# Performance work log

Measured on AMD Instinct MI355X. Metric: run time of the kernel, lower is better.

The kernel has to match this reference:

```python
import jax, jax.numpy as jnp
import numpy as np
import math

B, CIN, CH, H, W = 4, 64, 32, 64, 64
M_CH, DEPTH, K = 4, 3, 8
NPF = CIN // 2  # num_pos_feats per axis; pos channels = 2*NPF = CIN
TEMPERATURE = 10000.0


def sine_pos(h, w, npf, temperature=TEMPERATURE):
    # PositionEmbeddingSine with normalize=False; cumsum of ones == arange(1, n+1)
    y_embed = jnp.arange(1, h + 1, dtype=jnp.float32)
    x_embed = jnp.arange(1, w + 1, dtype=jnp.float32)
    dim_t = jnp.arange(npf, dtype=jnp.float32)
    dim_t = temperature ** (2.0 * jnp.floor(dim_t / 2.0) / npf)
    pos_x = jnp.broadcast_to(x_embed[None, :, None] / dim_t, (h, w, npf))
    pos_y = jnp.broadcast_to(y_embed[:, None, None] / dim_t, (h, w, npf))

    def interleave(p):
        return jnp.stack([jnp.sin(p[..., 0::2]), jnp.cos(p[..., 1::2])], axis=-1).reshape(h, w, npf)

    pos = jnp.concatenate([interleave(pos_y), interleave(pos_x)], axis=-1)  # (h,w,2*npf)
    return jnp.transpose(pos, (2, 0, 1))  # (2*npf, h, w)


def conv2d(x, wgt, bias, pad):
    y = jax.lax.conv_general_dilated(
        x, wgt, window_strides=(1, 1), padding=[(pad, pad), (pad, pad)],
        dimension_numbers=('NCHW', 'OIHW', 'NCHW'))
    return y + bias[None, :, None, None]


def setup_inputs() -> dict:
    key = jax.random.key(0)
    ks = jax.random.split(key, 13)
    s = 0.05
    return {
        'f':    jax.random.normal(ks[0], (B, CH, H, W), jnp.float32),
        'map':  jax.random.normal(ks[1], (B, 1, 32, 32), jnp.float32),
        'f_q':  jax.random.normal(ks[2], (B, CIN, H, W), jnp.float32),
        'f_k':  jax.random.normal(ks[3], (B, CIN, H, W), jnp.float32),
        'm_k':  jax.random.normal(ks[4], (B, 1, 32, 32), jnp.float32),
        'wq':   jax.random.normal(ks[5], (M_CH, CIN), jnp.float32) * s,
        'wk':   jax.random.normal(ks[6], (M_CH, CIN), jnp.float32) * s,
        'w_in':  jax.random.normal(ks[7], (CH, CH, 1, 1), jnp.float32) * s,
        'b_in':  jax.random.normal(ks[8], (CH,), jnp.float32) * s,
        'w_mid': jax.random.normal(ks[9], (DEPTH, CH, CH, 3, 3), jnp.float32) * s,
        'b_mid': jax.random.normal(ks[10], (DEPTH, CH), jnp.float32) * s,
        'w_out': jax.random.normal(ks[11], (1, CH, 3, 3), jnp.float32) * s,
        'b_out': jax.random.normal(ks[12], (1,), jnp.float32) * s,
    }


def reference(f, map, f_q, f_k, m_k, wq, wk, w_in, b_in, w_mid, b_mid, w_out, b_out):
    b, c, h, w = f_q.shape
    hf, wf = f.shape[2], f.shape[3]
    # self.ret: bilinear resize to f's spatial size (align_corners=False)
    map_r = jax.image.resize(map, (b, 1, hf, wf), method='bilinear')
    m_k_r = jax.image.resize(m_k, (b, 1, hf, wf), method='bilinear')

    pos = sine_pos(h, w, NPF)[None]  # (1, CIN, h, w); same for pos_emb_h/pos_emb_l
    fq_emb = f_q + pos
    fk_emb = f_k + pos

    # 1x1 convs == channel matmuls
    query = jnp.einsum('mc,bchw->bhwm', wq, fq_emb).reshape(b, h * w, M_CH)  # (b, N, m)
    key_t = jnp.einsum('mc,bchw->bmhw', wk, fk_emb).reshape(b, M_CH, h * w)  # (b, m, N)

    sim = jnp.einsum('bqm,bmk->bqk', query, key_t)   # (b, N, N)
    sim = jax.nn.softmax(sim, axis=-2)                # softmax over query axis (dim=-2)

    value = (jnp.exp(m_k_r) / math.e).reshape(b, 1, h * w)  # broadcast over query axis
    context = sim * value
    context_k, _ = jax.lax.top_k(context, K)          # (b, N, K) over last (key) axis
    context_m = jnp.mean(context_k, axis=-1)          # (b, N)
    corrected_map = context_m.reshape(b, 1, h, w)

    corrected_map = corrected_map * map_r + map_r
    rmap = 1.0 - jax.nn.sigmoid(corrected_map)

    x = rmap * f  # broadcast over channel dim
    x = conv2d(x, w_in, b_in, 0)
    for i in range(DEPTH):
        x = jax.nn.relu(conv2d(x, w_mid[i], b_mid[i], 1))
    out = conv2d(x, w_out, b_out, 1) + corrected_map
    return (x, out, corrected_map)
```

## Files before the change

kernel.cpp:

```cpp
#include <hip/hip_runtime.h>
#include <hip/hip_bf16.h>
#include <math.h>

#define BB 4
#define CIN 64
#define CH 32
#define NN 4096
#define NQCH 32
#define LOG2E 1.4426950408889634f
#define L2_10K 13.287712379549449f

#define Q4_OFF     1024
#define K4_OFF     66560
#define CV_OFF     132096
#define RMAP_OFF   148480
#define CMAPF_OFF  164864
#define CPSUM_OFF  181248
#define T8_OFF     705536
#define XA_OFF     4899840
#define XB_OFF     5424128

#define OUT_X_OFF   0
#define OUT_O_OFF   524288
#define OUT_CM_OFF  540672

#define CE(x, y) { float ce_lo = fminf(x, y); y = fmaxf(x, y); x = ce_lo; }
#define CED(x, y) { float ce_hi = fmaxf(x, y); y = fminf(x, y); x = ce_hi; }

#define SORT8(a0,a1,a2,a3,a4,a5,a6,a7) \
    CE(a0,a1); CE(a2,a3); CE(a4,a5); CE(a6,a7); \
    CE(a0,a2); CE(a1,a3); CE(a4,a6); CE(a5,a7); \
    CE(a1,a2); CE(a5,a6); \
    CE(a0,a4); CE(a1,a5); CE(a2,a6); CE(a3,a7); \
    CE(a2,a4); CE(a3,a5); \
    CE(a1,a2); CE(a3,a4); CE(a5,a6);

#define BITONIC8(a0,a1,a2,a3,a4,a5,a6,a7) \
    CE(a0,a4); CE(a1,a5); CE(a2,a6); CE(a3,a7); \
    CE(a0,a2); CE(a1,a3); CE(a4,a6); CE(a5,a7); \
    CE(a0,a1); CE(a2,a3); CE(a4,a5); CE(a6,a7);

__device__ __forceinline__ float bilin32(const float* src, int b, int y, int x) {
    float sy = 0.5f * y - 0.25f;
    float sx = 0.5f * x - 0.25f;
    float fy0 = floorf(sy), fx0 = floorf(sx);
    int y0 = (int)fy0, x0 = (int)fx0;
    float fy = sy - fy0, fx = sx - fx0;
    int y0c = min(max(y0, 0), 31), y1c = min(max(y0 + 1, 0), 31);
    int x0c = min(max(x0, 0), 31), x1c = min(max(x0 + 1, 0), 31);
    const float* p = src + b * 1024;
    float v00 = p[y0c * 32 + x0c], v01 = p[y0c * 32 + x1c];
    float v10 = p[y1c * 32 + x0c], v11 = p[y1c * 32 + x1c];
    float v0 = v00 + fx * (v01 - v00);
    float v1 = v10 + fx * (v11 - v10);
    return v0 + fy * (v1 - v0);
}

__global__ __launch_bounds__(512) void k1_qk(
        const float* __restrict__ fq, const float* __restrict__ fk,
        const float* __restrict__ wq, const float* __restrict__ wk,
        float* __restrict__ Q4, float* __restrict__ K4) {
    __shared__ float wqs[256], wks[256];
    __shared__ float pp[1024];
    __shared__ float red[512][9];
    int tid = threadIdx.x;
    if (tid < 256) { wqs[tid] = wq[tid]; wks[tid] = wk[tid]; }
    __syncthreads();
    if (tid < 64) {
        float coord = (float)(tid + 1);
        float qy[4] = {0,0,0,0}, qx[4] = {0,0,0,0}, ky[4] = {0,0,0,0}, kx[4] = {0,0,0,0};
        for (int c = 0; c < 32; ++c) {
            float e = (2.0f * (float)(c >> 1)) * (1.0f / 32.0f);
            float ang = coord * exp2f(-e * L2_10K);
            float pr = (c & 1) ? cosf(ang) : sinf(ang);
            #pragma unroll
            for (int m = 0; m < 4; ++m) {
                qy[m] += wqs[m * 64 + c] * pr;
                qx[m] += wqs[m * 64 + 32 + c] * pr;
                ky[m] += wks[m * 64 + c] * pr;
                kx[m] += wks[m * 64 + 32 + c] * pr;
            }
        }
        #pragma unroll
        for (int m = 0; m < 4; ++m) {
            pp[0 * 256 + m * 64 + tid] = qy[m];
            pp[1 * 256 + m * 64 + tid] = qx[m];
            pp[2 * 256 + m * 64 + tid] = ky[m];
            pp[3 * 256 + m * 64 + tid] = kx[m];
        }
    }
    int qi = tid & 63, g = tid >> 6;
    int gid = blockIdx.x * 64 + qi;
    int b = gid >> 12, hw = gid & 4095;
    const float* fqb = fq + (size_t)b * CIN * NN + hw;
    const float* fkb = fk + (size_t)b * CIN * NN + hw;
    float aq[4] = {0,0,0,0}, ak[4] = {0,0,0,0};
    int c0 = g * 8;
    #pragma unroll
    for (int c = c0; c < c0 + 8; ++c) {
        float vq = fqb[c * NN];
        float vk = fkb[c * NN];
        #pragma unroll
        for (int m = 0; m < 4; ++m) {
            aq[m] += wqs[m * 64 + c] * vq;
            ak[m] += wks[m * 64 + c] * vk;
        }
    }
    #pragma unroll
    for (int m = 0; m < 4; ++m) { red[tid][m] = aq[m]; red[tid][4 + m] = ak[m]; }
    __syncthreads();
    if (tid < 64) {
        int y = hw >> 6, x = hw & 63;
        float q4[4], k4[4];
        #pragma unroll
        for (int m = 0; m < 4; ++m) {
            float sq = 0.0f, sk = 0.0f;
            #pragma unroll
            for (int j = 0; j < 8; ++j) {
                sq += red[tid + 64 * j][m];
                sk += red[tid + 64 * j][4 + m];
            }
            q4[m] = LOG2E * (sq + pp[0 * 256 + m * 64 + y] + pp[1 * 256 + m * 64 + x]);
            k4[m] = sk + pp[2 * 256 + m * 64 + y] + pp[3 * 256 + m * 64 + x];
        }
        ((float4*)Q4)[gid] = make_float4(q4[0], q4[1], q4[2], q4[3]);
        ((float4*)K4)[gid] = make_float4(k4[0], k4[1], k4[2], k4[3]);
    }
}

__global__ void k2a_colstats(const float* __restrict__ Q4, const float* __restrict__ K4,
                             float* __restrict__ cpsum) {
    int blk = blockIdx.x;
    int kblk = blk & 7;   blk >>= 3;
    int qch  = blk & 31;  blk >>= 5;
    int b    = blk;
    int tid = threadIdx.x;
    const float4* Qg = (const float4*)Q4 + b * NN + qch * 128;
    int k0 = kblk * 512 + tid;
    float4 kva = ((const float4*)K4)[b * NN + k0];
    float4 kvb = ((const float4*)K4)[b * NN + k0 + 256];
    float sa = 0.0f, sb = 0.0f;
    #pragma unroll 8
    for (int i = 0; i < 128; ++i) {
        float4 q = Qg[i];
        float da = fmaf(q.x, kva.x, fmaf(q.y, kva.y, fmaf(q.z, kva.z, q.w * kva.w)));
        float db = fmaf(q.x, kvb.x, fmaf(q.y, kvb.y, fmaf(q.z, kvb.z, q.w * kvb.w)));
        sa += exp2f(da);
        sb += exp2f(db);
    }
    cpsum[(b * NQCH + qch) * NN + k0] = sa;
    cpsum[(b * NQCH + qch) * NN + k0 + 256] = sb;
}

__global__ void k2b_cmerge(const float* __restrict__ cpsum,
                           const float* __restrict__ m_k, float* __restrict__ cvals) {
    int gid = blockIdx.x * 256 + threadIdx.x;
    int b = gid >> 12, k = gid & 4095;
    float S = 0.0f;
    #pragma unroll
    for (int j = 0; j < NQCH; ++j) S += cpsum[(b * NQCH + j) * NN + k];
    float mk = bilin32(m_k, b, k >> 6, k & 63);
    cvals[gid] = LOG2E * (mk - 1.0f) - log2f(S);
}

__global__ __launch_bounds__(256) void k3a_scan(
        const float* __restrict__ Q4, const float* __restrict__ K4,
        const float* __restrict__ cvals, float* __restrict__ t8) {
    int blk = blockIdx.x;
    int kc = blk & 31;  blk >>= 5;
    int g4 = blk & 15;  blk >>= 4;
    int b  = blk;
    int tid = threadIdx.x;
    int wave = tid >> 6, lane = tid & 63;
    int qrow = (g4 * 4 + wave) * 64 + lane;
    float4 qv = ((const float4*)Q4)[b * NN + qrow];
    const float4* Kb = (const float4*)K4 + b * NN + kc * 128;
    const float* cb = cvals + b * NN + kc * 128;

    float t0=-1e30f,t1=-1e30f,t2=-1e30f,t3=-1e30f;
    float t4=-1e30f,t5=-1e30f,t6=-1e30f,t7=-1e30f;

    for (int i0 = 0; i0 < 128; i0 += 16) {
        float4 cA = *(const float4*)(cb + i0);
        float4 cB = *(const float4*)(cb + i0 + 4);
        float4 cC = *(const float4*)(cb + i0 + 8);
        float4 cD = *(const float4*)(cb + i0 + 12);
        float4 k0 = Kb[i0 + 0];  float4 k1 = Kb[i0 + 1];
        float4 k2 = Kb[i0 + 2];  float4 k3 = Kb[i0 + 3];
        float4 k4 = Kb[i0 + 4];  float4 k5 = Kb[i0 + 5];
        float4 k6 = Kb[i0 + 6];  float4 k7 = Kb[i0 + 7];
        float s0 = fmaf(qv.x,k0.x, fmaf(qv.y,k0.y, fmaf(qv.z,k0.z, qv.w*k0.w))) + cA.x;
        float s1 = fmaf(qv.x,k1.x, fmaf(qv.y,k1.y, fmaf(qv.z,k1.z, qv.w*k1.w))) + cA.y;
        float s2 = fmaf(qv.x,k2.x, fmaf(qv.y,k2.y, fmaf(qv.z,k2.z, qv.w*k2.w))) + cA.z;
        float s3 = fmaf(qv.x,k3.x, fmaf(qv.y,k3.y, fmaf(qv.z,k3.z, qv.w*k3.w))) + cA.w;
        float s4 = fmaf(qv.x,k4.x, fmaf(qv.y,k4.y, fmaf(qv.z,k4.z, qv.w*k4.w))) + cB.x;
        float s5 = fmaf(qv.x,k5.x, fmaf(qv.y,k5.y, fmaf(qv.z,k5.z, qv.w*k5.w))) + cB.y;
        float s6 = fmaf(qv.x,k6.x, fmaf(qv.y,k6.y, fmaf(qv.z,k6.z, qv.w*k6.w))) + cB.z;
        float s7 = fmaf(qv.x,k7.x, fmaf(qv.y,k7.y, fmaf(qv.z,k7.z, qv.w*k7.w))) + cB.w;
        float4 k8 = Kb[i0 + 8];  float4 k9 = Kb[i0 + 9];
        float4 kA = Kb[i0 + 10]; float4 kB = Kb[i0 + 11];
        float4 kC = Kb[i0 + 12]; float4 kD = Kb[i0 + 13];
        float4 kE = Kb[i0 + 14]; float4 kF = Kb[i0 + 15];
        float s8 = fmaf(qv.x,k8.x, fmaf(qv.y,k8.y, fmaf(qv.z,k8.z, qv.w*k8.w))) + cC.x;
        float s9 = fmaf(qv.x,k9.x, fmaf(qv.y,k9.y, fmaf(qv.z,k9.z, qv.w*k9.w))) + cC.y;
        float sA = fmaf(qv.x,kA.x, fmaf(qv.y,kA.y, fmaf(qv.z,kA.z, qv.w*kA.w))) + cC.z;
        float sB = fmaf(qv.x,kB.x, fmaf(qv.y,kB.y, fmaf(qv.z,kB.z, qv.w*kB.w))) + cC.w;
        float sC = fmaf(qv.x,kC.x, fmaf(qv.y,kC.y, fmaf(qv.z,kC.z, qv.w*kC.w))) + cD.x;
        float sD = fmaf(qv.x,kD.x, fmaf(qv.y,kD.y, fmaf(qv.z,kD.z, qv.w*kD.w))) + cD.y;
        float sE = fmaf(qv.x,kE.x, fmaf(qv.y,kE.y, fmaf(qv.z,kE.z, qv.w*kE.w))) + cD.z;
        float sF = fmaf(qv.x,kF.x, fmaf(qv.y,kF.y, fmaf(qv.z,kF.z, qv.w*kF.w))) + cD.w;
        float bm = fmaxf(
            fmaxf(fmaxf(fmaxf(s0,s1), fmaxf(s2,s3)), fmaxf(fmaxf(s4,s5), fmaxf(s6,s7))),
            fmaxf(fmaxf(fmaxf(s8,s9), fmaxf(sA,sB)), fmaxf(fmaxf(sC,sD), fmaxf(sE,sF))));
        if (bm > t0) {
            SORT8(s0,s1,s2,s3,s4,s5,s6,s7);
            SORT8(s8,s9,sA,sB,sC,sD,sE,sF);
            float u0 = fmaxf(s0, sF), u1 = fmaxf(s1, sE);
            float u2 = fmaxf(s2, sD), u3 = fmaxf(s3, sC);
            float u4 = fmaxf(s4, sB), u5 = fmaxf(s5, sA);
            float u6 = fmaxf(s6, s9), u7 = fmaxf(s7, s8);
            BITONIC8(u0,u1,u2,u3,u4,u5,u6,u7);
            t0 = fmaxf(t0, u7); t1 = fmaxf(t1, u6); t2 = fmaxf(t2, u5); t3 = fmaxf(t3, u4);
            t4 = fmaxf(t4, u3); t5 = fmaxf(t5, u2); t6 = fmaxf(t6, u1); t7 = fmaxf(t7, u0);
            BITONIC8(t0,t1,t2,t3,t4,t5,t6,t7);
        }
    }
    float* o = t8 + ((size_t)(b * NN + qrow)) * 256 + kc * 8;
    o[0] = t0; o[1] = t1; o[2] = t2; o[3] = t3;
    o[4] = t4; o[5] = t5; o[6] = t6; o[7] = t7;
}

__global__ void k3b_merge(const float* __restrict__ t8, const float* __restrict__ mapin,
                          float* __restrict__ rmap, float* __restrict__ cmapf,
                          float* __restrict__ outp) {
    int tid = threadIdx.x;
    int qid = blockIdx.x * 4 + (tid >> 6);
    int lane = tid & 63;
    const float* p = t8 + (size_t)qid * 256;
    float a = p[lane], bq = p[lane + 64], c = p[lane + 128], d = p[lane + 192];
    CED(a, c); CED(bq, d); CED(a, bq); CED(c, d); CED(bq, c);
    float sm = 0.0f;
    #pragma unroll
    for (int r = 0; r < 8; ++r) {
        float m = a;
        int ln = lane;
        #pragma unroll
        for (int off = 32; off >= 1; off >>= 1) {
            float om = __shfl_xor(m, off);
            int ol = __shfl_xor(ln, off);
            if (om > m || (om == m && ol < ln)) { m = om; ln = ol; }
        }
        sm += exp2f(m);
        if (lane == ln) { a = bq; bq = c; c = d; d = -1e30f; }
    }
    if (lane == 0) {
        float cmv = sm * 0.125f;
        int b = qid >> 12, hw = qid & 4095;
        float mr = bilin32(mapin, b, hw >> 6, hw & 63);
        float cm = cmv * mr + mr;
        rmap[qid] = 1.0f / (1.0f + __expf(cm));
        cmapf[qid] = cm;
        outp[OUT_CM_OFF + qid] = cm;
    }
}

__global__ void k4_conv1(const float* __restrict__ f, const float* __restrict__ rmap,
                         const float* __restrict__ w_in, const float* __restrict__ b_in,
                         float* __restrict__ xout) {
    __shared__ float ws_[1024];
    __shared__ float bs[32];
    int tid = threadIdx.x;
    for (int i = tid; i < 1024; i += 256) ws_[i] = w_in[i];
    if (tid < 32) bs[tid] = b_in[tid];
    __syncthreads();
    int gid = blockIdx.x * 256 + tid;
    int hw = gid & 4095;
    int og = (gid >> 12) & 7;
    int b  = gid >> 15;
    float rm = rmap[b * NN + hw];
    float acc[4];
    #pragma unroll
    for (int j = 0; j < 4; ++j) acc[j] = bs[og * 4 + j];
    const float* fb = f + (size_t)b * CH * NN + hw;
    for (int i = 0; i < 32; ++i) {
        float v = fb[i * NN] * rm;
        #pragma unroll
        for (int j = 0; j < 4; ++j) acc[j] += ws_[(og * 4 + j) * 32 + i] * v;
    }
    float* xo = xout + (size_t)b * CH * NN + (og * 4) * NN + hw;
    #pragma unroll
    for (int j = 0; j < 4; ++j) xo[j * NN] = acc[j];
}

__global__ void k5_conv3(const float* __restrict__ xin, const float* __restrict__ w,
                         const float* __restrict__ bias, float* __restrict__ xout,
                         float* __restrict__ outx) {
    __shared__ float tile[32][324];
    __shared__ float wsm[1152];
    __shared__ float bsm[4];
    int blk = blockIdx.x;
    int og = blk & 7;  blk >>= 3;
    int tx = blk & 3;  blk >>= 2;
    int ty = blk & 3;  blk >>= 2;
    int b  = blk;
    int tid = threadIdx.x;
    for (int i = tid; i < 1152; i += 256) wsm[i] = w[og * 1152 + i];
    if (tid < 4) bsm[tid] = bias[og * 4 + tid];
    int y0 = ty * 16 - 1, x0 = tx * 16 - 1;
    for (int i = tid; i < 32 * 324; i += 256) {
        int c = i / 324, r = i % 324;
        int yy = r / 18, xx = r % 18;
        int gy = y0 + yy, gx = x0 + xx;
        float v = 0.0f;
        if (gy >= 0 && gy < 64 && gx >= 0 && gx < 64)
            v = xin[((size_t)b * CH + c) * NN + gy * 64 + gx];
        tile[c][r] = v;
    }
    __syncthreads();
    int py = tid >> 4, px = tid & 15;
    float acc[4];
    #pragma unroll
    for (int j = 0; j < 4; ++j) acc[j] = bsm[j];
    for (int i = 0; i < 32; ++i) {
        const float* tr = &tile[i][py * 18 + px];
        float v00 = tr[0],  v01 = tr[1],  v02 = tr[2];
        float v10 = tr[18], v11 = tr[19], v12 = tr[20];
        float v20 = tr[36], v21 = tr[37], v22 = tr[38];
        #pragma unroll
        for (int j = 0; j < 4; ++j) {
            const float* wj = &wsm[j * 288 + i * 9];
            acc[j] += v00 * wj[0] + v01 * wj[1] + v02 * wj[2]
                    + v10 * wj[3] + v11 * wj[4] + v12 * wj[5]
                    + v20 * wj[6] + v21 * wj[7] + v22 * wj[8];
        }
    }
    size_t base = (size_t)b * CH * NN + (size_t)(og * 4) * NN
                + (ty * 16 + py) * 64 + tx * 16 + px;
    #pragma unroll
    for (int j = 0; j < 4; ++j) {
        float r_ = fmaxf(acc[j], 0.0f);
        xout[base + j * NN] = r_;
        if (outx) outx[base + j * NN] = r_;
    }
}

__global__ void k6_convout(const float* __restrict__ xin, const float* __restrict__ w_out,
                           const float* __restrict__ b_out, const float* __restrict__ cmapf,
                           float* __restrict__ outp) {
    __shared__ float wsm[288];
    __shared__ float red[256];
    int tid = threadIdx.x;
    for (int i = tid; i < 288; i += 256) wsm[i] = w_out[i];
    int pxi = tid & 63, g = tid >> 6;
    int gid = blockIdx.x * 64 + pxi;
    int b = gid >> 12, hw = gid & 4095;
    int y = hw >> 6, x = hw & 63;
    __syncthreads();
    float acc = 0.0f;
    int c0 = g * 8;
    for (int i = c0; i < c0 + 8; ++i) {
        const float* xi = xin + ((size_t)b * CH + i) * NN;
        #pragma unroll
        for (int ky = 0; ky < 3; ++ky) {
            int gy = y + ky - 1;
            if (gy < 0 || gy > 63) continue;
            #pragma unroll
            for (int kx = 0; kx < 3; ++kx) {
                int gx = x + kx - 1;
                if (gx < 0 || gx > 63) continue;
                acc += xi[gy * 64 + gx] * wsm[i * 9 + ky * 3 + kx];
            }
        }
    }
    red[tid] = acc;
    __syncthreads();
    if (tid < 64) {
        float a = red[tid] + red[tid + 64] + red[tid + 128] + red[tid + 192]
                + b_out[0] + cmapf[gid];
        outp[OUT_O_OFF + gid] = a;
    }
}

extern "C" void kernel_launch(void* const* d_in, const int* in_sizes, int n_in,
                              void* d_out, int out_size, void* d_ws, size_t ws_size,
                              hipStream_t stream) {
    const float* f     = (const float*)d_in[0];
    const float* mapin = (const float*)d_in[1];
    const float* f_q   = (const float*)d_in[2];
    const float* f_k   = (const float*)d_in[3];
    const float* m_k   = (const float*)d_in[4];
    const float* wq    = (const float*)d_in[5];
    const float* wk    = (const float*)d_in[6];
    const float* w_in  = (const float*)d_in[7];
    const float* b_in  = (const float*)d_in[8];
    const float* w_mid = (const float*)d_in[9];
    const float* b_mid = (const float*)d_in[10];
    const float* w_out = (const float*)d_in[11];
    const float* b_out = (const float*)d_in[12];
    float* outp = (float*)d_out;
    float* ws = (float*)d_ws;

    float* Q4    = ws + Q4_OFF;
    float* K4    = ws + K4_OFF;
    float* CV    = ws + CV_OFF;
    float* CPSUM = ws + CPSUM_OFF;
    float* RMAP  = ws + RMAP_OFF;
    float* CMAPF = ws + CMAPF_OFF;
    float* T8    = ws + T8_OFF;
    float* XA    = ws + XA_OFF;
    float* XB    = ws + XB_OFF;

    k1_qk<<<256, 512, 0, stream>>>(f_q, f_k, wq, wk, Q4, K4);
    k2a_colstats<<<BB * NQCH * 8, 256, 0, stream>>>(Q4, K4, CPSUM);
    k2b_cmerge<<<64, 256, 0, stream>>>(CPSUM, m_k, CV);
    k3a_scan<<<BB * 16 * 32, 256, 0, stream>>>(Q4, K4, CV, T8);
    k3b_merge<<<BB * NN / 4, 256, 0, stream>>>(T8, mapin, RMAP, CMAPF, outp);
    k4_conv1<<<512, 256, 0, stream>>>(f, RMAP, w_in, b_in, XA);
    k5_conv3<<<512, 256, 0, stream>>>(XA, w_mid + 0 * 9216, b_mid + 0 * 32, XB, (float*)0);
    k5_conv3<<<512, 256, 0, stream>>>(XB, w_mid + 1 * 9216, b_mid + 1 * 32, XA, (float*)0);
    k5_conv3<<<512, 256, 0, stream>>>(XA, w_mid + 2 * 9216, b_mid + 2 * 32, XB, outp + OUT_X_OFF);
    k6_convout<<<256, 256, 0, stream>>>(XB, w_out, b_out, CMAPF, outp);
}
```

Baseline: 202.2 us.

## Precompute 1x1 conv in QK kernel, fuse rmap scaling into first 3x3 conv, inline column merge

Uses the linearity of the 1x1 input conv over the per-pixel rmap scale: W·(rmap*f) = rmap*(W·f). The unscaled product W·f is computed in extra blocks of the first kernel, which do not depend on attention. The first 3x3 conv then applies rmap and the bias while it loads its tile, so the standalone conv1 kernel goes away. The column-merge kernel is also folded into the scan kernel, where each block recomputes its 128 column constants into shared memory. This cuts two launches and one full activation round trip, at the cost of redundant cpsum reads across the 16 query groups.

```diff
diff --git a/kernel.cpp b/kernel.cpp
--- a/kernel.cpp
+++ b/kernel.cpp
@@ -12,13 +12,13 @@
 
 #define Q4_OFF     1024
 #define K4_OFF     66560
-#define CV_OFF     132096
-#define RMAP_OFF   148480
-#define CMAPF_OFF  164864
-#define CPSUM_OFF  181248
-#define T8_OFF     705536
-#define XA_OFF     4899840
-#define XB_OFF     5424128
+#define RMAP_OFF   132096
+#define CMAPF_OFF  148480
+#define CPSUM_OFF  164864
+#define T8_OFF     689152
+#define G_OFF      4883456
+#define XA_OFF     5407744
+#define XB_OFF     5932032
 
 #define OUT_X_OFF   0
 #define OUT_O_OFF   524288
@@ -56,75 +56,97 @@
     return v0 + fy * (v1 - v0);
 }
 
-__global__ __launch_bounds__(512) void k1_qk(
+__global__ __launch_bounds__(512) void k1g(
         const float* __restrict__ fq, const float* __restrict__ fk,
         const float* __restrict__ wq, const float* __restrict__ wk,
-        float* __restrict__ Q4, float* __restrict__ K4) {
+        const float* __restrict__ f, const float* __restrict__ w_in,
+        float* __restrict__ Q4, float* __restrict__ K4, float* __restrict__ G) {
     __shared__ float wqs[256], wks[256];
     __shared__ float pp[1024];
     __shared__ float red[512][9];
     int tid = threadIdx.x;
-    if (tid < 256) { wqs[tid] = wq[tid]; wks[tid] = wk[tid]; }
-    __syncthreads();
-    if (tid < 64) {
-        float coord = (float)(tid + 1);
-        float qy[4] = {0,0,0,0}, qx[4] = {0,0,0,0}, ky[4] = {0,0,0,0}, kx[4] = {0,0,0,0};
-        for (int c = 0; c < 32; ++c) {
-            float e = (2.0f * (float)(c >> 1)) * (1.0f / 32.0f);
-            float ang = coord * exp2f(-e * L2_10K);
-            float pr = (c & 1) ? cosf(ang) : sinf(ang);
+    if (blockIdx.x < 256) {
+        if (tid < 256) { wqs[tid] = wq[tid]; wks[tid] = wk[tid]; }
+        __syncthreads();
+        if (tid < 64) {
+            float coord = (float)(tid + 1);
+            float qy[4] = {0,0,0,0}, qx[4] = {0,0,0,0}, ky[4] = {0,0,0,0}, kx[4] = {0,0,0,0};
+            for (int c = 0; c < 32; ++c) {
+                float e = (2.0f * (float)(c >> 1)) * (1.0f / 32.0f);
+                float ang = coord * exp2f(-e * L2_10K);
+                float pr = (c & 1) ? cosf(ang) : sinf(ang);
+                #pragma unroll
+                for (int m = 0; m < 4; ++m) {
+                    qy[m] += wqs[m * 64 + c] * pr;
+                    qx[m] += wqs[m * 64 + 32 + c] * pr;
+                    ky[m] += wks[m * 64 + c] * pr;
+                    kx[m] += wks[m * 64 + 32 + c] * pr;
+                }
+            }
             #pragma unroll
             for (int m = 0; m < 4; ++m) {
-                qy[m] += wqs[m * 64 + c] * pr;
-                qx[m] += wqs[m * 64 + 32 + c] * pr;
-                ky[m] += wks[m * 64 + c] * pr;
-                kx[m] += wks[m * 64 + 32 + c] * pr;
+                pp[0 * 256 + m * 64 + tid] = qy[m];
+                pp[1 * 256 + m * 64 + tid] = qx[m];
+                pp[2 * 256 + m * 64 + tid] = ky[m];
+                pp[3 * 256 + m * 64 + tid] = kx[m];
             }
         }
-        #pragma unroll
-        for (int m = 0; m < 4; ++m) {
-            pp[0 * 256 + m * 64 + tid] = qy[m];
-            pp[1 * 256 + m * 64 + tid] = qx[m];
-            pp[2 * 256 + m * 64 + tid] = ky[m];
-            pp[3 * 256 + m * 64 + tid] = kx[m];
-        }
-    }
-    int qi = tid & 63, g = tid >> 6;
-    int gid = blockIdx.x * 64 + qi;
-    int b = gid >> 12, hw = gid & 4095;
-    const float* fqb = fq + (size_t)b * CIN * NN + hw;
-    const float* fkb = fk + (size_t)b * CIN * NN + hw;
-    float aq[4] = {0,0,0,0}, ak[4] = {0,0,0,0};
-    int c0 = g * 8;
-    #pragma unroll
-    for (int c = c0; c < c0 + 8; ++c) {
-        float vq = fqb[c * NN];
-        float vk = fkb[c * NN];
-        #pragma unroll
-        for (int m = 0; m < 4; ++m) {
-            aq[m] += wqs[m * 64 + c] * vq;
-            ak[m] += wks[m * 64 + c] * vk;
-        }
-    }
-    #pragma unroll
-    for (int m = 0; m < 4; ++m) { red[tid][m] = aq[m]; red[tid][4 + m] = ak[m]; }
-    __syncthreads();
-    if (tid < 64) {
-        int y = hw >> 6, x = hw & 63;
-        float q4[4], k4[4];
-        #pragma unroll
-        for (int m = 0; m < 4; ++m) {
-            float sq = 0.0f, sk = 0.0f;
+        int qi = tid & 63, g = tid >> 6;
+        int gid = blockIdx.x * 64 + qi;
+        int b = gid >> 12, hw = gid & 4095;
+        const float* fqb = fq + (size_t)b * CIN * NN + hw;
+        const float* fkb = fk + (size_t)b * CIN * NN + hw;
+        float aq[4] = {0,0,0,0}, ak[4] = {0,0,0,0};
+        int c0 = g * 8;
+        #pragma unroll
+        for (int c = c0; c < c0 + 8; ++c) {
+            float vq = fqb[c * NN];
+            float vk = fkb[c * NN];
             #pragma unroll
-            for (int j = 0; j < 8; ++j) {
-                sq += red[tid + 64 * j][m];
-                sk += red[tid + 64 * j][4 + m];
+            for (int m = 0; m < 4; ++m) {
+                aq[m] += wqs[m * 64 + c] * vq;
+                ak[m] += wks[m * 64 + c] * vk;
             }
-            q4[m] = LOG2E * (sq + pp[0 * 256 + m * 64 + y] + pp[1 * 256 + m * 64 + x]);
-            k4[m] = sk + pp[2 * 256 + m * 64 + y] + pp[3 * 256 + m * 64 + x];
-        }
-        ((float4*)Q4)[gid] = make_float4(q4[0], q4[1], q4[2], q4[3]);
-        ((float4*)K4)[gid] = make_float4(k4[0], k4[1], k4[2], k4[3]);
+        }
+        #pragma unroll
+        for (int m = 0; m < 4; ++m) { red[tid][m] = aq[m]; red[tid][4 + m] = ak[m]; }
+        __syncthreads();
+        if (tid < 64) {
+            int y = hw >> 6, x = hw & 63;
+            float q4[4], k4[4];
+            #pragma unroll
+            for (int m = 0; m < 4; ++m) {
+                float sq = 0.0f, sk = 0.0f;
+                #pragma unroll
+                for (int j = 0; j < 8; ++j) {
+                    sq += red[tid + 64 * j][m];
+                    sk += red[tid + 64 * j][4 + m];
+                }
+                q4[m] = LOG2E * (sq + pp[0 * 256 + m * 64 + y] + pp[1 * 256 + m * 64 + x]);
+                k4[m] = sk + pp[2 * 256 + m * 64 + y] + pp[3 * 256 + m * 64 + x];
+            }
+            ((float4*)Q4)[gid] = make_float4(q4[0], q4[1], q4[2], q4[3]);
+            ((float4*)K4)[gid] = make_float4(k4[0], k4[1], k4[2], k4[3]);
+        }
+    } else {
+        if (tid < 1024) {  }
+        float* ws_ = pp;
+        for (int i = tid; i < 1024; i += 512) ws_[i] = w_in[i];
+        __syncthreads();
+        int gid = (blockIdx.x - 256) * 512 + tid;
+        int hw = gid & 4095;
+        int og = (gid >> 12) & 7;
+        int b  = gid >> 15;
+        float acc[4] = {0.0f, 0.0f, 0.0f, 0.0f};
+        const float* fb = f + (size_t)b * CH * NN + hw;
+        for (int i = 0; i < 32; ++i) {
+            float v = fb[i * NN];
+            #pragma unroll
+            for (int j = 0; j < 4; ++j) acc[j] += ws_[(og * 4 + j) * 32 + i] * v;
+        }
+        float* go = G + (size_t)b * CH * NN + (og * 4) * NN + hw;
+        #pragma unroll
+        for (int j = 0; j < 4; ++j) go[j * NN] = acc[j];
     }
 }
 
@@ -152,39 +174,39 @@
     cpsum[(b * NQCH + qch) * NN + k0 + 256] = sb;
 }
 
-__global__ void k2b_cmerge(const float* __restrict__ cpsum,
-                           const float* __restrict__ m_k, float* __restrict__ cvals) {
-    int gid = blockIdx.x * 256 + threadIdx.x;
-    int b = gid >> 12, k = gid & 4095;
-    float S = 0.0f;
-    #pragma unroll
-    for (int j = 0; j < NQCH; ++j) S += cpsum[(b * NQCH + j) * NN + k];
-    float mk = bilin32(m_k, b, k >> 6, k & 63);
-    cvals[gid] = LOG2E * (mk - 1.0f) - log2f(S);
-}
-
 __global__ __launch_bounds__(256) void k3a_scan(
         const float* __restrict__ Q4, const float* __restrict__ K4,
-        const float* __restrict__ cvals, float* __restrict__ t8) {
+        const float* __restrict__ cpsum, const float* __restrict__ m_k,
+        float* __restrict__ t8) {
+    __shared__ float cvs[128];
     int blk = blockIdx.x;
     int kc = blk & 31;  blk >>= 5;
     int g4 = blk & 15;  blk >>= 4;
     int b  = blk;
     int tid = threadIdx.x;
+    if (tid < 128) {
+        int k = kc * 128 + tid;
+        float S = 0.0f;
+        #pragma unroll
+        for (int j = 0; j < NQCH; ++j) S += cpsum[(b * NQCH + j) * NN + k];
+        float mk = bilin32(m_k, b, k >> 6, k & 63);
+        cvs[tid] = LOG2E * (mk - 1.0f) - log2f(S);
+    }
+    __syncthreads();
+
     int wave = tid >> 6, lane = tid & 63;
     int qrow = (g4 * 4 + wave) * 64 + lane;
     float4 qv = ((const float4*)Q4)[b * NN + qrow];
     const float4* Kb = (const float4*)K4 + b * NN + kc * 128;
-    const float* cb = cvals + b * NN + kc * 128;
 
     float t0=-1e30f,t1=-1e30f,t2=-1e30f,t3=-1e30f;
     float t4=-1e30f,t5=-1e30f,t6=-1e30f,t7=-1e30f;
 
     for (int i0 = 0; i0 < 128; i0 += 16) {
-        float4 cA = *(const float4*)(cb + i0);
-        float4 cB = *(const float4*)(cb + i0 + 4);
-        float4 cC = *(const float4*)(cb + i0 + 8);
-        float4 cD = *(const float4*)(cb + i0 + 12);
+        float4 cA = *(const float4*)(cvs + i0);
+        float4 cB = *(const float4*)(cvs + i0 + 4);
+        float4 cC = *(const float4*)(cvs + i0 + 8);
+        float4 cD = *(const float4*)(cvs + i0 + 12);
         float4 k0 = Kb[i0 + 0];  float4 k1 = Kb[i0 + 1];
         float4 k2 = Kb[i0 + 2];  float4 k3 = Kb[i0 + 3];
         float4 k4 = Kb[i0 + 4];  float4 k5 = Kb[i0 + 5];
@@ -264,32 +286,59 @@
     }
 }
 
-__global__ void k4_conv1(const float* __restrict__ f, const float* __restrict__ rmap,
-                         const float* __restrict__ w_in, const float* __restrict__ b_in,
-                         float* __restrict__ xout) {
-    __shared__ float ws_[1024];
-    __shared__ float bs[32];
-    int tid = threadIdx.x;
-    for (int i = tid; i < 1024; i += 256) ws_[i] = w_in[i];
-    if (tid < 32) bs[tid] = b_in[tid];
-    __syncthreads();
-    int gid = blockIdx.x * 256 + tid;
-    int hw = gid & 4095;
-    int og = (gid >> 12) & 7;
-    int b  = gid >> 15;
-    float rm = rmap[b * NN + hw];
+__global__ void k5a_conv3(const float* __restrict__ G, const float* __restrict__ rmap,
+                          const float* __restrict__ b_in, const float* __restrict__ w,
+                          const float* __restrict__ bias, float* __restrict__ xout) {
+    __shared__ float tile[32][324];
+    __shared__ float wsm[1152];
+    __shared__ float bsm[4];
+    __shared__ float bin_s[32];
+    int blk = blockIdx.x;
+    int og = blk & 7;  blk >>= 3;
+    int tx = blk & 3;  blk >>= 2;
+    int ty = blk & 3;  blk >>= 2;
+    int b  = blk;
+    int tid = threadIdx.x;
+    for (int i = tid; i < 1152; i += 256) wsm[i] = w[og * 1152 + i];
+    if (tid < 4) bsm[tid] = bias[og * 4 + tid];
+    if (tid < 32) bin_s[tid] = b_in[tid];
+    __syncthreads();
+    int y0 = ty * 16 - 1, x0 = tx * 16 - 1;
+    const float* rb = rmap + b * NN;
+    for (int i = tid; i < 32 * 324; i += 256) {
+        int c = i / 324, r = i % 324;
+        int yy = r / 18, xx = r % 18;
+        int gy = y0 + yy, gx = x0 + xx;
+        float v = 0.0f;
+        if (gy >= 0 && gy < 64 && gx >= 0 && gx < 64) {
+            int p = gy * 64 + gx;
+            v = fmaf(G[((size_t)b * CH + c) * NN + p], rb[p], bin_s[c]);
+        }
+        tile[c][r] = v;
+    }
+    __syncthreads();
+    int py = tid >> 4, px = tid & 15;
     float acc[4];
     #pragma unroll
-    for (int j = 0; j < 4; ++j) acc[j] = bs[og * 4 + j];
-    const float* fb = f + (size_t)b * CH * NN + hw;
+    for (int j = 0; j < 4; ++j) acc[j] = bsm[j];
     for (int i = 0; i < 32; ++i) {
-        float v = fb[i * NN] * rm;
-        #pragma unroll
-        for (int j = 0; j < 4; ++j) acc[j] += ws_[(og * 4 + j) * 32 + i] * v;
-    }
-    float* xo = xout + (size_t)b * CH * NN + (og * 4) * NN + hw;
+        const float* tr = &tile[i][py * 18 + px];
+        float v00 = tr[0],  v01 = tr[1],  v02 = tr[2];
+        float v10 = tr[18], v11 = tr[19], v12 = tr[20];
+        float v20 = tr[36], v21 = tr[37], v22 = tr[38];
+        #pragma unroll
+        for (int j = 0; j < 4; ++j) {
+            const float* wj = &wsm[j * 288 + i * 9];
+            acc[j] += v00 * wj[0] + v01 * wj[1] + v02 * wj[2]
+                    + v10 * wj[3] + v11 * wj[4] + v12 * wj[5]
+                    + v20 * wj[6] + v21 * wj[7] + v22 * wj[8];
+        }
+    }
+    size_t base = (size_t)b * CH * NN + (size_t)(og * 4) * NN
+                + (ty * 16 + py) * 64 + tx * 16 + px;
     #pragma unroll
-    for (int j = 0; j < 4; ++j) xo[j * NN] = acc[j];
+    for (int j = 0; j < 4; ++j)
+        xout[base + j * NN] = fmaxf(acc[j], 0.0f);
 }
 
 __global__ void k5_conv3(const float* __restrict__ xin, const float* __restrict__ w,
@@ -402,21 +451,19 @@
 
     float* Q4    = ws + Q4_OFF;
     float* K4    = ws + K4_OFF;
-    float* CV    = ws + CV_OFF;
-    float* CPSUM = ws + CPSUM_OFF;
     float* RMAP  = ws + RMAP_OFF;
     float* CMAPF = ws + CMAPF_OFF;
+    float* CPSUM = ws + CPSUM_OFF;
     float* T8    = ws + T8_OFF;
+    float* G     = ws + G_OFF;
     float* XA    = ws + XA_OFF;
     float* XB    = ws + XB_OFF;
 
-    k1_qk<<<256, 512, 0, stream>>>(f_q, f_k, wq, wk, Q4, K4);
+    k1g<<<512, 512, 0, stream>>>(f_q, f_k, wq, wk, f, w_in, Q4, K4, G);
     k2a_colstats<<<BB * NQCH * 8, 256, 0, stream>>>(Q4, K4, CPSUM);
-    k2b_cmerge<<<64, 256, 0, stream>>>(CPSUM, m_k, CV);
-    k3a_scan<<<BB * 16 * 32, 256, 0, stream>>>(Q4, K4, CV, T8);
+    k3a_scan<<<BB * 16 * 32, 256, 0, stream>>>(Q4, K4, CPSUM, m_k, T8);
     k3b_merge<<<BB * NN / 4, 256, 0, stream>>>(T8, mapin, RMAP, CMAPF, outp);
-    k4_conv1<<<512, 256, 0, stream>>>(f, RMAP, w_in, b_in, XA);
-    k5_conv3<<<512, 256, 0, stream>>>(XA, w_mid + 0 * 9216, b_mid + 0 * 32, XB, (float*)0);
+    k5a_conv3<<<512, 256, 0, stream>>>(G, RMAP, b_in, w_mid + 0 * 9216, b_mid + 0 * 32, XB);
     k5_conv3<<<512, 256, 0, stream>>>(XB, w_mid + 1 * 9216, b_mid + 1 * 32, XA, (float*)0);
     k5_conv3<<<512, 256, 0, stream>>>(XA, w_mid + 2 * 9216, b_mid + 2 * 32, XB, outp + OUT_X_OFF);
     k6_convout<<<256, 256, 0, stream>>>(XB, w_out, b_out, CMAPF, outp);
```

New measurement: 196.3 us. 1.03x faster.
